# Kernel optimization log

Hardware: AMD Instinct MI355X
Metric: run time of the kernel (lower is better)

## Reference

```python
import jax, jax.numpy as jnp
import numpy as np

N, E = 50000, 800000
IN_DIM, HID, OUT_DIM, HEADS = 256, 128, 128, 2
EPS_BN = 1e-5


def _glorot(key, shape):
    fan_in, fan_out = shape[0], shape[-1]
    lim = float(np.sqrt(6.0 / (fan_in + fan_out)))
    return jax.random.uniform(key, shape, jnp.float32, -lim, lim)


def setup_inputs() -> dict:
    key = jax.random.key(0)
    ks = jax.random.split(key, 12)
    x = jax.random.normal(ks[0], (N, IN_DIM), jnp.float32)
    edge_index = jax.random.randint(ks[1], (2, E), 0, N, jnp.int64)
    return {
        "x": x,
        "edge_index": edge_index,
        # layer 1 (heads=2, concat)
        "W1": _glorot(ks[2], (IN_DIM, HEADS * HID)),
        "att_src1": _glorot(ks[3], (HEADS, HID)),
        "att_dst1": _glorot(ks[4], (HEADS, HID)),
        "b1": jnp.zeros((HEADS * HID,), jnp.float32),
        "g1": jnp.ones((HEADS * HID,), jnp.float32),
        "be1": jnp.zeros((HEADS * HID,), jnp.float32),
        # layer 2 (heads=1, no concat)
        "W2": _glorot(ks[5], (HEADS * HID, OUT_DIM)),
        "att_src2": _glorot(ks[6], (1, OUT_DIM)),
        "att_dst2": _glorot(ks[7], (1, OUT_DIM)),
        "b2": jnp.zeros((OUT_DIM,), jnp.float32),
        "g2": jnp.ones((OUT_DIM,), jnp.float32),
        "be2": jnp.zeros((OUT_DIM,), jnp.float32),
    }


def gat_conv(x, src, dst, W, att_src, att_dst, bias, heads, out_ch, concat):
    """PyG GATConv forward (dropout=identity at eval). Messages flow src->dst,
    softmax over incoming edges of dst, sum-aggregate."""
    h = (x @ W).reshape(-1, heads, out_ch)             # [N, H, C]
    a_s = jnp.einsum('nhc,hc->nh', h, att_src)          # [N, H]
    a_d = jnp.einsum('nhc,hc->nh', h, att_dst)
    e = jax.nn.leaky_relu(a_s[src] + a_d[dst], 0.2)     # [E, H]
    m = jax.ops.segment_max(e, dst, num_segments=N)     # [N, H]
    m = jnp.where(jnp.isfinite(m), m, 0.0)
    w = jnp.exp(e - m[dst])                             # [E, H]
    denom = jax.ops.segment_sum(w, dst, num_segments=N) # [N, H]
    alpha = w / (denom[dst] + 1e-16)                    # [E, H]
    msg = h[src] * alpha[:, :, None]                    # [E, H, C]
    out = jax.ops.segment_sum(msg, dst, num_segments=N) # [N, H, C]
    if concat:
        out = out.reshape(-1, heads * out_ch)
    else:
        out = out.mean(axis=1)
    return out + bias


def batchnorm_relu(x, gamma, beta):
    mu = x.mean(axis=0)
    var = x.var(axis=0)  # biased, as used for normalization in torch BN
    xn = (x - mu) * jax.lax.rsqrt(var + EPS_BN)
    return jax.nn.relu(xn * gamma + beta)


def reference(x, edge_index, W1, att_src1, att_dst1, b1, g1, be1,
              W2, att_src2, att_dst2, b2, g2, be2):
    src, dst = edge_index[0], edge_index[1]
    h = gat_conv(x, src, dst, W1, att_src1, att_dst1, b1, HEADS, HID, True)
    h = batchnorm_relu(h, g1, be1)
    h = gat_conv(h, src, dst, W2, att_src2, att_dst2, b2, 1, OUT_DIM, False)
    h = batchnorm_relu(h, g2, be2)
    return h
```

## Files before the change

### kernel.cpp

```cpp
#include <hip/hip_runtime.h>
#include <math.h>

#define IN_DIM 256
#define EPS_BN 1e-5f
#define NS 16

typedef __attribute__((ext_vector_type(8))) short short8v;
typedef __attribute__((ext_vector_type(4))) float f32x4;

__device__ __forceinline__ float lrelu(float v) { return v > 0.f ? v : 0.2f * v; }

__device__ __forceinline__ unsigned short f2bf(float f) {
    unsigned int u = __float_as_uint(f);
    u += 0x7fffu + ((u >> 16) & 1u);
    return (unsigned short)(u >> 16);
}
__device__ __forceinline__ float bf2f(unsigned short s) {
    return __uint_as_float((unsigned int)s << 16);
}

__device__ __forceinline__ void gld16(const void* g, void* l) {
    __builtin_amdgcn_global_load_lds((const __attribute__((address_space(1))) void*)g,
                                     (__attribute__((address_space(3))) void*)l, 16, 0, 0);
}

__device__ __forceinline__ int edge_at(const void* ei, int is64, long long i) {
    if (is64) return (int)((const long long*)ei)[i];
    return ((const int*)ei)[i];
}

__global__ __launch_bounds__(256) void prep_kernel(const float* __restrict__ x,
                                                   unsigned short* __restrict__ xb, long long n8,
                                                   const float* __restrict__ W1,
                                                   unsigned short* __restrict__ Wt1,
                                                   const float* __restrict__ W2,
                                                   unsigned short* __restrict__ Wt2,
                                                   const unsigned int* __restrict__ eiw,
                                                   int* __restrict__ flag, long long nwords) {
    __shared__ int nz;
    long long nbx = (n8 + 255) / 256;
    long long b = blockIdx.x;
    if (b < nbx) {
        long long i = b * 256 + threadIdx.x;
        if (i < n8) {
            const float4* p = (const float4*)(x + i * 8);
            float4 v0 = p[0], v1 = p[1];
            ushort4 o0, o1;
            o0.x = f2bf(v0.x); o0.y = f2bf(v0.y); o0.z = f2bf(v0.z); o0.w = f2bf(v0.w);
            o1.x = f2bf(v1.x); o1.y = f2bf(v1.y); o1.z = f2bf(v1.z); o1.w = f2bf(v1.w);
            *(ushort4*)(xb + i * 8) = o0;
            *(ushort4*)(xb + i * 8 + 4) = o1;
        }
        return;
    }
    b -= nbx;
    if (b < 256) {
        int idx = (int)b * 256 + threadIdx.x;
        int c = idx >> 8, k = idx & 255;
        Wt1[idx] = f2bf(W1[(long long)k * 256 + c]);
        return;
    }
    b -= 256;
    if (b < 128) {
        int idx = (int)b * 256 + threadIdx.x;
        int c = idx >> 8, k = idx & 255;
        Wt2[idx] = f2bf(W2[(long long)k * 128 + c]);
        return;
    }
    if (threadIdx.x == 0) nz = 0;
    __syncthreads();
    int cnt = 0;
    for (int i = 0; i < 4; i++) {
        long long idx = 2LL * (threadIdx.x + i * 256) + 1;
        if (idx < nwords && eiw[idx] != 0u) cnt++;
    }
    if (cnt) atomicAdd(&nz, 1);
    __syncthreads();
    if (threadIdx.x == 0) flag[0] = (nz == 0) ? 1 : 0;
}

__global__ void count_deg_kernel(const void* __restrict__ ei, const int* __restrict__ flag,
                                 int* __restrict__ deg, int E_) {
    int is64 = flag[0];
    int i = blockIdx.x * 256 + threadIdx.x;
    if (i < E_) {
        int d = edge_at(ei, is64, (long long)E_ + i);
        atomicAdd(&deg[d], 1);
    }
}

__global__ __launch_bounds__(256) void scan_partial_kernel(const int* __restrict__ deg,
                                                           int* __restrict__ bsum, int n) {
    __shared__ int sh[256];
    int t = threadIdx.x;
    int i = blockIdx.x * 256 + t;
    sh[t] = (i < n) ? deg[i] : 0;
    __syncthreads();
    for (int off = 128; off >= 1; off >>= 1) {
        if (t < off) sh[t] += sh[t + off];
        __syncthreads();
    }
    if (t == 0) bsum[blockIdx.x] = sh[0];
}

__global__ __launch_bounds__(256) void scan_write_kernel(const int* __restrict__ deg,
                                                         const int* __restrict__ bsum,
                                                         int* __restrict__ rowptr,
                                                         int* __restrict__ ctr, int n, int nb) {
    __shared__ int sh[256];
    __shared__ int base_sh;
    int t = threadIdx.x;
    int b = blockIdx.x;
    sh[t] = (t < b) ? bsum[t] : 0;
    __syncthreads();
    for (int off = 128; off >= 1; off >>= 1) {
        if (t < off) sh[t] += sh[t + off];
        __syncthreads();
    }
    if (t == 0) base_sh = sh[0];
    __syncthreads();
    int i = b * 256 + t;
    int d = (i < n) ? deg[i] : 0;
    sh[t] = d;
    __syncthreads();
    for (int off = 1; off < 256; off <<= 1) {
        int u = (t >= off) ? sh[t - off] : 0;
        __syncthreads();
        sh[t] += u;
        __syncthreads();
    }
    if (i < n) {
        int v = base_sh + sh[t] - d;
        rowptr[i] = v;
        ctr[i] = v;
    }
    if (b == nb - 1 && t == 255) rowptr[n] = base_sh + sh[255];
}

__global__ void scatter_kernel(const void* __restrict__ ei, const int* __restrict__ flag,
                               int* __restrict__ ctr, int* __restrict__ srcs, int E_) {
    int is64 = flag[0];
    int i = blockIdx.x * 256 + threadIdx.x;
    if (i < E_) {
        int s = edge_at(ei, is64, i);
        int d = edge_at(ei, is64, (long long)E_ + i);
        int pos = atomicAdd(&ctr[d], 1);
        srcs[pos] = s;
    }
}

template <int NCOL, int NH, bool FUSEBN>
__global__ __launch_bounds__(256) void gemm_mfma_kernel(const unsigned short* __restrict__ Ab,
                                                        const unsigned short* __restrict__ Wt,
                                                        unsigned short* __restrict__ C,
                                                        const float* __restrict__ att_s,
                                                        const float* __restrict__ att_d,
                                                        float* __restrict__ a_s,
                                                        float* __restrict__ a_d, int M,
                                                        const float* __restrict__ bnsh,
                                                        const float* __restrict__ gamma,
                                                        const float* __restrict__ beta) {
    __shared__ unsigned short B_lds[64 * 256];
    __shared__ unsigned short A_lds[128 * 64];
    __shared__ float scs[FUSEBN ? 256 : 1];
    __shared__ float shs[FUSEBN ? 256 : 1];
    const int t = threadIdx.x;
    const int w = t >> 6, l = t & 63;
    const int row0 = blockIdx.x * 128;
    const int col0 = blockIdx.y * 64;

    {
        const char* wb = (const char*)Wt + (size_t)col0 * 512;
#pragma unroll
        for (int it = 0; it < 8; ++it) {
            int q = w * 8 + it;
            int i = q * 64 + l;
            int r = i >> 5;
            int cs = (i & 31) ^ (r & 7);
            gld16(wb + (size_t)r * 512 + cs * 16, (char*)B_lds + q * 1024);
        }
    }

    short8v nxt[4];
    const char* ab = (const char*)Ab + (size_t)row0 * 512;

    if (FUSEBN) {
        {
            int c = t;
            float s = 0.f, q = 0.f;
#pragma unroll
            for (int sh = 0; sh < NS; sh++) { s += bnsh[sh * 512 + c]; q += bnsh[sh * 512 + 256 + c]; }
            float invN = 1.f / (float)M;
            float mu = s * invN;
            float var = q * invN - mu * mu;
            float sc = rsqrtf(var + EPS_BN) * gamma[c];
            scs[c] = sc;
            shs[c] = beta[c] - mu * sc;
        }
#pragma unroll
        for (int it = 0; it < 4; ++it) {
            int i = it * 256 + t;
            int r = i >> 3, g = i & 7;
            int gr = row0 + r;
            nxt[it] = (gr < M) ? *(const short8v*)(Ab + (size_t)gr * 256 + g * 8)
                               : (short8v)(short)0;
        }
        __syncthreads();
#pragma unroll
        for (int it = 0; it < 4; ++it) {
            int i = it * 256 + t;
            int r = i >> 3, g = i & 7;
            int kb = g * 8;
            float4 s0 = *(const float4*)&scs[kb], s1 = *(const float4*)&scs[kb + 4];
            float4 h0 = *(const float4*)&shs[kb], h1 = *(const float4*)&shs[kb + 4];
            short8v v = nxt[it];
            short8v ov;
            ov[0] = (short)f2bf(fmaxf(bf2f((unsigned short)v[0]) * s0.x + h0.x, 0.f));
            ov[1] = (short)f2bf(fmaxf(bf2f((unsigned short)v[1]) * s0.y + h0.y, 0.f));
            ov[2] = (short)f2bf(fmaxf(bf2f((unsigned short)v[2]) * s0.z + h0.z, 0.f));
            ov[3] = (short)f2bf(fmaxf(bf2f((unsigned short)v[3]) * s0.w + h0.w, 0.f));
            ov[4] = (short)f2bf(fmaxf(bf2f((unsigned short)v[4]) * s1.x + h1.x, 0.f));
            ov[5] = (short)f2bf(fmaxf(bf2f((unsigned short)v[5]) * s1.y + h1.y, 0.f));
            ov[6] = (short)f2bf(fmaxf(bf2f((unsigned short)v[6]) * s1.z + h1.z, 0.f));
            ov[7] = (short)f2bf(fmaxf(bf2f((unsigned short)v[7]) * s1.w + h1.w, 0.f));
            *(short8v*)((char*)A_lds + r * 128 + ((g ^ (r & 7)) << 4)) = ov;
        }
    } else {
#pragma unroll
        for (int it = 0; it < 4; ++it) {
            int q = w * 4 + it;
            int i = q * 64 + l;
            int r = i >> 3;
            int cs = (i & 7) ^ (r & 7);
            gld16(ab + (size_t)r * 512 + cs * 16, (char*)A_lds + q * 1024);
        }
    }
    __syncthreads();

    const int rl = l & 15, kg = l >> 4;
    f32x4 acc0[4], acc1[4];
#pragma unroll
    for (int i = 0; i < 4; ++i) { acc0[i] = (f32x4)(0.f); acc1[i] = (f32x4)(0.f); }

    const int ar0 = w * 32 + rl, ar1 = ar0 + 16;
    const int aswz = (ar0 & 7) << 4;

    for (int c = 0; c < 4; ++c) {
        if (FUSEBN && c < 3) {
#pragma unroll
            for (int it = 0; it < 4; ++it) {
                int i = it * 256 + t;
                int r = i >> 3, g = i & 7;
                int gr = row0 + r;
                nxt[it] = (gr < M) ? *(const short8v*)(Ab + (size_t)gr * 256 + (c + 1) * 64 + g * 8)
                                   : (short8v)(short)0;
            }
        }
#pragma unroll
        for (int s = 0; s < 2; ++s) {
            short8v a0 = *(const short8v*)((const char*)A_lds +
                          ((ar0 * 128 + s * 64 + kg * 16) ^ aswz));
            short8v a1 = *(const short8v*)((const char*)A_lds +
                          ((ar1 * 128 + s * 64 + kg * 16) ^ aswz));
#pragma unroll
            for (int ct = 0; ct < 4; ++ct) {
                int br = ct * 16 + rl;
                short8v bfr = *(const short8v*)((const char*)B_lds +
                               ((br * 512 + c * 128 + s * 64 + kg * 16) ^ ((br & 7) << 4)));
                acc0[ct] = __builtin_amdgcn_mfma_f32_16x16x32_bf16(a0, bfr, acc0[ct], 0, 0, 0);
                acc1[ct] = __builtin_amdgcn_mfma_f32_16x16x32_bf16(a1, bfr, acc1[ct], 0, 0, 0);
            }
        }
        __syncthreads();
        if (c < 3) {
            if (FUSEBN) {
#pragma unroll
                for (int it = 0; it < 4; ++it) {
                    int i = it * 256 + t;
                    int r = i >> 3, g = i & 7;
                    int kb = (c + 1) * 64 + g * 8;
                    float4 s0 = *(const float4*)&scs[kb], s1 = *(const float4*)&scs[kb + 4];
                    float4 h0 = *(const float4*)&shs[kb], h1 = *(const float4*)&shs[kb + 4];
                    short8v v = nxt[it];
                    short8v ov;
                    ov[0] = (short)f2bf(fmaxf(bf2f((unsigned short)v[0]) * s0.x + h0.x, 0.f));
                    ov[1] = (short)f2bf(fmaxf(bf2f((unsigned short)v[1]) * s0.y + h0.y, 0.f));
                    ov[2] = (short)f2bf(fmaxf(bf2f((unsigned short)v[2]) * s0.z + h0.z, 0.f));
                    ov[3] = (short)f2bf(fmaxf(bf2f((unsigned short)v[3]) * s0.w + h0.w, 0.f));
                    ov[4] = (short)f2bf(fmaxf(bf2f((unsigned short)v[4]) * s1.x + h1.x, 0.f));
                    ov[5] = (short)f2bf(fmaxf(bf2f((unsigned short)v[5]) * s1.y + h1.y, 0.f));
                    ov[6] = (short)f2bf(fmaxf(bf2f((unsigned short)v[6]) * s1.z + h1.z, 0.f));
                    ov[7] = (short)f2bf(fmaxf(bf2f((unsigned short)v[7]) * s1.w + h1.w, 0.f));
                    *(short8v*)((char*)A_lds + r * 128 + ((g ^ (r & 7)) << 4)) = ov;
                }
            } else {
#pragma unroll
                for (int it = 0; it < 4; ++it) {
                    int q = w * 4 + it;
                    int i = q * 64 + l;
                    int r = i >> 3;
                    int cs = (i & 7) ^ (r & 7);
                    gld16(ab + (size_t)r * 512 + (c + 1) * 128 + cs * 16, (char*)A_lds + q * 1024);
                }
            }
            __syncthreads();
        }
    }

#pragma unroll
    for (int ct = 0; ct < 4; ++ct) {
#pragma unroll
        for (int r = 0; r < 4; ++r) {
            int gr0 = row0 + w * 32 + kg * 4 + r;
            if (gr0 < M) C[(long long)gr0 * NCOL + col0 + ct * 16 + rl] = f2bf(acc0[ct][r]);
            int gr1 = gr0 + 16;
            if (gr1 < M) C[(long long)gr1 * NCOL + col0 + ct * 16 + rl] = f2bf(acc1[ct][r]);
        }
    }

    float asp0[4] = {}, adp0[4] = {}, asp1[4] = {}, adp1[4] = {};
#pragma unroll
    for (int ct = 0; ct < 4; ++ct) {
        int col = col0 + ct * 16 + rl;
        float vs = att_s[col], vd = att_d[col];
#pragma unroll
        for (int r = 0; r < 4; ++r) {
            asp0[r] += acc0[ct][r] * vs; adp0[r] += acc0[ct][r] * vd;
            asp1[r] += acc1[ct][r] * vs; adp1[r] += acc1[ct][r] * vd;
        }
    }
#pragma unroll
    for (int off = 1; off < 16; off <<= 1) {
#pragma unroll
        for (int r = 0; r < 4; ++r) {
            asp0[r] += __shfl_xor(asp0[r], off);
            adp0[r] += __shfl_xor(adp0[r], off);
            asp1[r] += __shfl_xor(asp1[r], off);
            adp1[r] += __shfl_xor(adp1[r], off);
        }
    }
    if (rl == 0) {
        int head = (NH == 2) ? (col0 >> 7) : 0;
#pragma unroll
        for (int r = 0; r < 4; ++r) {
            int gr0 = row0 + w * 32 + kg * 4 + r;
            if (gr0 < M) {
                atomicAdd(&a_s[gr0 * NH + head], asp0[r]);
                atomicAdd(&a_d[gr0 * NH + head], adp0[r]);
            }
            int gr1 = gr0 + 16;
            if (gr1 < M) {
                atomicAdd(&a_s[gr1 * NH + head], asp1[r]);
                atomicAdd(&a_d[gr1 * NH + head], adp1[r]);
            }
        }
    }
}

__global__ __launch_bounds__(256) void aggregate1_kernel(const unsigned short* __restrict__ h,
                                                         const int* __restrict__ rowptr,
                                                         const int* __restrict__ srcs,
                                                         const float* __restrict__ a_s,
                                                         const float* __restrict__ a_d,
                                                         const float* __restrict__ bias,
                                                         unsigned short* __restrict__ out,
                                                         float* __restrict__ bnsh, int Nn) {
    __shared__ float sw_lds[4 * 256];
    __shared__ float ssum[4][256];
    __shared__ float ssq[4][256];
    const int t = threadIdx.x;
    const int wid = t >> 6, lane = t & 63;
    const int n = blockIdx.x * 4 + wid;
    const int colb = (lane & 31) * 8;
    if (lane < 32) {
#pragma unroll
        for (int j = 0; j < 8; j++) { ssum[wid][colb + j] = 0.f; ssq[wid][colb + j] = 0.f; }
    }
    if (n < Nn) {
        float* wbase = &sw_lds[wid * 256];
        int beg = rowptr[n], end = rowptr[n + 1];
        float2 adv = *(const float2*)&a_d[(size_t)n * 2];
        float ad0 = adv.x, ad1 = adv.y;
        const int hh = (lane >> 4) & 1;
        const int eb = lane >> 5;
        float acc[8] = {0.f, 0.f, 0.f, 0.f, 0.f, 0.f, 0.f, 0.f};
        float den = 0.f, m0 = -1e30f, m1 = -1e30f;

        for (int cb = beg; cb < end; cb += 64) {
            int cnt = end - cb; if (cnt > 64) cnt = 64;
            float e0 = -1e30f, e1 = -1e30f;
            int s_l = 0;
            if (lane < cnt) {
                s_l = srcs[cb + lane];
                float2 av = *(const float2*)&a_s[(size_t)s_l * 2];
                e0 = lrelu(av.x + ad0);
                e1 = lrelu(av.y + ad1);
            }
            float cm0 = e0, cm1 = e1;
            for (int off = 32; off >= 1; off >>= 1) {
                cm0 = fmaxf(cm0, __shfl_xor(cm0, off));
                cm1 = fmaxf(cm1, __shfl_xor(cm1, off));
            }
            if (cm0 > m0 || cm1 > m1) {
                float f0 = (cm0 > m0) ? __expf(m0 - cm0) : 1.f;
                float f1 = (cm1 > m1) ? __expf(m1 - cm1) : 1.f;
                m0 = fmaxf(m0, cm0); m1 = fmaxf(m1, cm1);
                float fo = hh ? f1 : f0;
#pragma unroll
                for (int j = 0; j < 8; j++) acc[j] *= fo;
                den *= fo;
            }
            if (lane < cnt) {
                *(float2*)&wbase[lane * 2] = make_float2(__int_as_float(s_l), __expf(e0 - m0));
                *(float2*)&wbase[128 + lane * 2] = make_float2(__int_as_float(s_l), __expf(e1 - m1));
            }
            int c = 0;
            for (; c + 8 <= cnt; c += 8) {
                float2 sw0 = *(const float2*)&wbase[hh * 128 + (c + eb) * 2];
                float2 sw1 = *(const float2*)&wbase[hh * 128 + (c + 2 + eb) * 2];
                float2 sw2 = *(const float2*)&wbase[hh * 128 + (c + 4 + eb) * 2];
                float2 sw3 = *(const float2*)&wbase[hh * 128 + (c + 6 + eb) * 2];
                short8v p0 = *(const short8v*)(h + ((size_t)__float_as_int(sw0.x) << 8) + colb);
                short8v p1 = *(const short8v*)(h + ((size_t)__float_as_int(sw1.x) << 8) + colb);
                short8v p2 = *(const short8v*)(h + ((size_t)__float_as_int(sw2.x) << 8) + colb);
                short8v p3 = *(const short8v*)(h + ((size_t)__float_as_int(sw3.x) << 8) + colb);
                den += sw0.y + sw1.y + sw2.y + sw3.y;
#pragma unroll
                for (int j = 0; j < 8; j++)
                    acc[j] += sw0.y * bf2f((unsigned short)p0[j]) + sw1.y * bf2f((unsigned short)p1[j])
                            + sw2.y * bf2f((unsigned short)p2[j]) + sw3.y * bf2f((unsigned short)p3[j]);
            }
            for (; c + 4 <= cnt; c += 4) {
                float2 sw0 = *(const float2*)&wbase[hh * 128 + (c + eb) * 2];
                float2 sw1 = *(const float2*)&wbase[hh * 128 + (c + 2 + eb) * 2];
                short8v p0 = *(const short8v*)(h + ((size_t)__float_as_int(sw0.x) << 8) + colb);
                short8v p1 = *(const short8v*)(h + ((size_t)__float_as_int(sw1.x) << 8) + colb);
                den += sw0.y + sw1.y;
#pragma unroll
                for (int j = 0; j < 8; j++)
                    acc[j] += sw0.y * bf2f((unsigned short)p0[j]) + sw1.y * bf2f((unsigned short)p1[j]);
            }
            for (; c < cnt; c += 2) {
                int e = c + eb;
                if (e < cnt) {
                    float2 sw0 = *(const float2*)&wbase[hh * 128 + e * 2];
                    short8v p0 = *(const short8v*)(h + ((size_t)__float_as_int(sw0.x) << 8) + colb);
                    den += sw0.y;
#pragma unroll
                    for (int j = 0; j < 8; j++) acc[j] += sw0.y * bf2f((unsigned short)p0[j]);
                }
            }
        }
        den += __shfl_xor(den, 32);
#pragma unroll
        for (int j = 0; j < 8; j++) acc[j] += __shfl_xor(acc[j], 32);
        if (lane < 32) {
            float inv = 1.f / (den + 1e-16f);
            float4 b0 = *(const float4*)&bias[colb];
            float4 b1 = *(const float4*)&bias[colb + 4];
            float of[8];
            of[0] = acc[0] * inv + b0.x; of[1] = acc[1] * inv + b0.y;
            of[2] = acc[2] * inv + b0.z; of[3] = acc[3] * inv + b0.w;
            of[4] = acc[4] * inv + b1.x; of[5] = acc[5] * inv + b1.y;
            of[6] = acc[6] * inv + b1.z; of[7] = acc[7] * inv + b1.w;
            short8v o;
#pragma unroll
            for (int j = 0; j < 8; j++) {
                o[j] = (short)f2bf(of[j]);
                ssum[wid][colb + j] = of[j];
                ssq[wid][colb + j] = of[j] * of[j];
            }
            *(short8v*)(out + ((size_t)n << 8) + colb) = o;
        }
    }
    __syncthreads();
    {
        int sh = blockIdx.x & (NS - 1);
        float s = ssum[0][t] + ssum[1][t] + ssum[2][t] + ssum[3][t];
        float q = ssq[0][t] + ssq[1][t] + ssq[2][t] + ssq[3][t];
        atomicAdd(&bnsh[sh * 512 + t], s);
        atomicAdd(&bnsh[sh * 512 + 256 + t], q);
    }
}

__global__ __launch_bounds__(256) void aggregate2_kernel(const unsigned short* __restrict__ h,
                                                         const int* __restrict__ rowptr,
                                                         const int* __restrict__ srcs,
                                                         const float* __restrict__ a_s,
                                                         const float* __restrict__ a_d,
                                                         const float* __restrict__ bias,
                                                         float* __restrict__ out,
                                                         float* __restrict__ bnsh, int Nn) {
    __shared__ float sw_lds[4 * 128];
    __shared__ float ssum[4][128];
    __shared__ float ssq[4][128];
    const int t = threadIdx.x;
    const int wid = t >> 6, lane = t & 63;
    const int n = blockIdx.x * 4 + wid;
    const int colb = (lane & 15) * 8;
    if (lane < 16) {
#pragma unroll
        for (int j = 0; j < 8; j++) { ssum[wid][colb + j] = 0.f; ssq[wid][colb + j] = 0.f; }
    }
    if (n < Nn) {
        float* wbase = &sw_lds[wid * 128];
        int beg = rowptr[n], end = rowptr[n + 1];
        float ad = a_d[n];
        const int eo = lane >> 4;
        float acc[8] = {0.f, 0.f, 0.f, 0.f, 0.f, 0.f, 0.f, 0.f};
        float den = 0.f, m = -1e30f;

        for (int cb = beg; cb < end; cb += 64) {
            int cnt = end - cb; if (cnt > 64) cnt = 64;
            float e_ = -1e30f;
            int s_l = 0;
            if (lane < cnt) {
                s_l = srcs[cb + lane];
                e_ = lrelu(a_s[s_l] + ad);
            }
            float cm = e_;
            for (int off = 32; off >= 1; off >>= 1) cm = fmaxf(cm, __shfl_xor(cm, off));
            if (cm > m) {
                float f = __expf(m - cm);
                m = cm;
#pragma unroll
                for (int j = 0; j < 8; j++) acc[j] *= f;
                den *= f;
            }
            if (lane < cnt)
                *(float2*)&wbase[lane * 2] = make_float2(__int_as_float(s_l), __expf(e_ - m));
            int c = 0;
            for (; c + 16 <= cnt; c += 16) {
                float2 sw0 = *(const float2*)&wbase[(c + eo) * 2];
                float2 sw1 = *(const float2*)&wbase[(c + 4 + eo) * 2];
                float2 sw2 = *(const float2*)&wbase[(c + 8 + eo) * 2];
                float2 sw3 = *(const float2*)&wbase[(c + 12 + eo) * 2];
                short8v p0 = *(const short8v*)(h + ((size_t)__float_as_int(sw0.x) << 7) + colb);
                short8v p1 = *(const short8v*)(h + ((size_t)__float_as_int(sw1.x) << 7) + colb);
                short8v p2 = *(const short8v*)(h + ((size_t)__float_as_int(sw2.x) << 7) + colb);
                short8v p3 = *(const short8v*)(h + ((size_t)__float_as_int(sw3.x) << 7) + colb);
                den += sw0.y + sw1.y + sw2.y + sw3.y;
#pragma unroll
                for (int j = 0; j < 8; j++)
                    acc[j] += sw0.y * bf2f((unsigned short)p0[j]) + sw1.y * bf2f((unsigned short)p1[j])
                            + sw2.y * bf2f((unsigned short)p2[j]) + sw3.y * bf2f((unsigned short)p3[j]);
            }
            for (; c + 8 <= cnt; c += 8) {
                float2 sw0 = *(const float2*)&wbase[(c + eo) * 2];
                float2 sw1 = *(const float2*)&wbase[(c + 4 + eo) * 2];
                short8v p0 = *(const short8v*)(h + ((size_t)__float_as_int(sw0.x) << 7) + colb);
                short8v p1 = *(const short8v*)(h + ((size_t)__float_as_int(sw1.x) << 7) + colb);
                den += sw0.y + sw1.y;
#pragma unroll
                for (int j = 0; j < 8; j++)
                    acc[j] += sw0.y * bf2f((unsigned short)p0[j]) + sw1.y * bf2f((unsigned short)p1[j]);
            }
            for (; c < cnt; c += 4) {
                int e = c + eo;
                if (e < cnt) {
                    float2 sw0 = *(const float2*)&wbase[e * 2];
                    short8v p0 = *(const short8v*)(h + ((size_t)__float_as_int(sw0.x) << 7) + colb);
                    den += sw0.y;
#pragma unroll
                    for (int j = 0; j < 8; j++) acc[j] += sw0.y * bf2f((unsigned short)p0[j]);
                }
            }
        }
        den += __shfl_xor(den, 16);
        den += __shfl_xor(den, 32);
#pragma unroll
        for (int j = 0; j < 8; j++) {
            acc[j] += __shfl_xor(acc[j], 16);
            acc[j] += __shfl_xor(acc[j], 32);
        }
        if (lane < 16) {
            float inv = 1.f / (den + 1e-16f);
            float4 b0 = *(const float4*)&bias[colb];
            float4 b1 = *(const float4*)&bias[colb + 4];
            float of[8];
            of[0] = acc[0] * inv + b0.x; of[1] = acc[1] * inv + b0.y;
            of[2] = acc[2] * inv + b0.z; of[3] = acc[3] * inv + b0.w;
            of[4] = acc[4] * inv + b1.x; of[5] = acc[5] * inv + b1.y;
            of[6] = acc[6] * inv + b1.z; of[7] = acc[7] * inv + b1.w;
#pragma unroll
            for (int j = 0; j < 8; j++) {
                ssum[wid][colb + j] = of[j];
                ssq[wid][colb + j] = of[j] * of[j];
            }
            float* ob = out + (size_t)n * 128 + colb;
            *(float4*)ob = make_float4(of[0], of[1], of[2], of[3]);
            *(float4*)(ob + 4) = make_float4(of[4], of[5], of[6], of[7]);
        }
    }
    __syncthreads();
    if (t < 128) {
        int sh = blockIdx.x & (NS - 1);
        float s = ssum[0][t] + ssum[1][t] + ssum[2][t] + ssum[3][t];
        atomicAdd(&bnsh[sh * 256 + t], s);
    } else {
        int c = t - 128;
        int sh = blockIdx.x & (NS - 1);
        float q = ssq[0][c] + ssq[1][c] + ssq[2][c] + ssq[3][c];
        atomicAdd(&bnsh[sh * 256 + 128 + c], q);
    }
}

__global__ __launch_bounds__(256) void bn_apply_final_kernel(float* __restrict__ x,
                                                             const float* __restrict__ bnsh,
                                                             const float* __restrict__ gamma,
                                                             const float* __restrict__ beta,
                                                             int Nn) {
    int t = threadIdx.x;
    int col = t & 127;
    float s = 0.f, q = 0.f;
#pragma unroll
    for (int sh = 0; sh < NS; sh++) { s += bnsh[sh * 256 + col]; q += bnsh[sh * 256 + 128 + col]; }
    float mu = s / (float)Nn;
    float var = q / (float)Nn - mu * mu;
    float sc = rsqrtf(var + EPS_BN) * gamma[col];
    float sh_ = beta[col] - mu * sc;
    int r0 = blockIdx.x * 2 + (t >> 7);
    int rs = gridDim.x * 2;
    for (int r = r0; r < Nn; r += rs) {
        size_t idx = (size_t)r * 128 + col;
        x[idx] = fmaxf(x[idx] * sc + sh_, 0.f);
    }
}

extern "C" void kernel_launch(void* const* d_in, const int* in_sizes, int n_in,
                              void* d_out, int out_size, void* d_ws, size_t ws_size,
                              hipStream_t stream) {
    const float* x        = (const float*)d_in[0];
    const void*  ei       = d_in[1];
    const float* W1       = (const float*)d_in[2];
    const float* att_src1 = (const float*)d_in[3];
    const float* att_dst1 = (const float*)d_in[4];
    const float* b1       = (const float*)d_in[5];
    const float* g1       = (const float*)d_in[6];
    const float* be1      = (const float*)d_in[7];
    const float* W2       = (const float*)d_in[8];
    const float* att_src2 = (const float*)d_in[9];
    const float* att_dst2 = (const float*)d_in[10];
    const float* b2       = (const float*)d_in[11];
    const float* g2       = (const float*)d_in[12];
    const float* be2      = (const float*)d_in[13];

    const int Nn = in_sizes[0] / IN_DIM;
    const int E_ = in_sizes[1] / 2;
    const int gb = (Nn + 127) / 128;
    const int Mpad = gb * 128 + 128;

    char* ws = (char*)d_ws;
    size_t o = 0;
    auto alloc = [&](size_t bytes) {
        size_t r = o;
        o += (bytes + 255) & ~(size_t)255;
        return r;
    };
    int* flag = (int*)(ws + alloc(4));
    size_t z0 = o;
    int*   deg   = (int*)(ws + alloc((size_t)Nn * 4));
    float* as1   = (float*)(ws + alloc((size_t)Nn * 2 * 4));
    float* ad1   = (float*)(ws + alloc((size_t)Nn * 2 * 4));
    float* as2   = (float*)(ws + alloc((size_t)Nn * 4));
    float* ad2   = (float*)(ws + alloc((size_t)Nn * 4));
    float* bn1sh = (float*)(ws + alloc((size_t)NS * 512 * 4));
    float* bn2sh = (float*)(ws + alloc((size_t)NS * 256 * 4));
    size_t z1 = o;
    int*   rowptr = (int*)(ws + alloc((size_t)(Nn + 1) * 4));
    int*   ctr    = (int*)(ws + alloc((size_t)Nn * 4));
    int*   srcs   = (int*)(ws + alloc((size_t)E_ * 4));
    int*   bsum   = (int*)(ws + alloc(256 * 4));
    unsigned short* Wt1  = (unsigned short*)(ws + alloc((size_t)256 * 256 * 2));
    unsigned short* Wt2  = (unsigned short*)(ws + alloc((size_t)128 * 256 * 2));
    unsigned short* xb   = (unsigned short*)(ws + alloc((size_t)Mpad * 256 * 2));
    unsigned short* x2b0 = (unsigned short*)(ws + alloc((size_t)Nn * 256 * 2));
    unsigned short* h1b  = (unsigned short*)(ws + alloc((size_t)Nn * 256 * 2));
    unsigned short* h2b  = (unsigned short*)(ws + alloc((size_t)Nn * 128 * 2));
    float* outf = (float*)d_out;

    hipMemsetAsync(ws + z0, 0, z1 - z0, stream);

    {
        long long n8 = (long long)Nn * 256 / 8;
        long long grid = (n8 + 255) / 256 + 256 + 128 + 1;
        prep_kernel<<<(int)grid, 256, 0, stream>>>(x, xb, n8, W1, Wt1, W2, Wt2,
                                                   (const unsigned int*)ei, flag,
                                                   (long long)2 * E_);
    }

    int eb = (E_ + 255) / 256;
    int nsb = (Nn + 255) / 256;
    count_deg_kernel<<<eb, 256, 0, stream>>>(ei, flag, deg, E_);
    scan_partial_kernel<<<nsb, 256, 0, stream>>>(deg, bsum, Nn);
    scan_write_kernel<<<nsb, 256, 0, stream>>>(deg, bsum, rowptr, ctr, Nn, nsb);
    scatter_kernel<<<eb, 256, 0, stream>>>(ei, flag, ctr, srcs, E_);

    int nb4 = (Nn + 3) / 4;

    gemm_mfma_kernel<256, 2, false><<<dim3(gb, 4), 256, 0, stream>>>(
        xb, Wt1, h1b, att_src1, att_dst1, as1, ad1, Nn, nullptr, nullptr, nullptr);
    aggregate1_kernel<<<nb4, 256, 0, stream>>>(h1b, rowptr, srcs, as1, ad1, b1, x2b0, bn1sh, Nn);

    gemm_mfma_kernel<128, 1, true><<<dim3(gb, 2), 256, 0, stream>>>(
        x2b0, Wt2, h2b, att_src2, att_dst2, as2, ad2, Nn, bn1sh, g1, be1);
    aggregate2_kernel<<<nb4, 256, 0, stream>>>(h2b, rowptr, srcs, as2, ad2, b2, outf, bn2sh, Nn);
    bn_apply_final_kernel<<<512, 256, 0, stream>>>(outf, bn2sh, g2, be2, Nn);
}
```

Baseline: 306.2 us.

## Use grid-stride persistent blocks in aggregation kernels with register BN partials

Both aggregation kernels become grid-stride loops over destination nodes, launched with a fixed 2048 blocks instead of one block per four nodes. Each lane keeps its batch-norm sum and sum-of-squares partials in registers across its nodes and does the LDS reduction and global atomics once per block. This cuts global atomic traffic on the sharded BN buffers by roughly 6x and removes per-node shared-memory staging. It reuses the weight LDS buffer for the reduction, which adds extra barriers at the end, and it can leave some blocks with more work than others when node degrees vary.

```diff
diff --git a/kernel.cpp b/kernel.cpp
--- a/kernel.cpp
+++ b/kernel.cpp
@@ -365,24 +365,20 @@
                                                          const float* __restrict__ bias,
                                                          unsigned short* __restrict__ out,
                                                          float* __restrict__ bnsh, int Nn) {
-    __shared__ float sw_lds[4 * 256];
-    __shared__ float ssum[4][256];
-    __shared__ float ssq[4][256];
+    __shared__ float sw_lds[4][256];
     const int t = threadIdx.x;
     const int wid = t >> 6, lane = t & 63;
-    const int n = blockIdx.x * 4 + wid;
+    const int hh = (lane >> 4) & 1;
+    const int eb = lane >> 5;
     const int colb = (lane & 31) * 8;
-    if (lane < 32) {
-#pragma unroll
-        for (int j = 0; j < 8; j++) { ssum[wid][colb + j] = 0.f; ssq[wid][colb + j] = 0.f; }
-    }
-    if (n < Nn) {
-        float* wbase = &sw_lds[wid * 256];
+    float* wbase = sw_lds[wid];
+    float bnsum[8] = {}, bnsq[8] = {};
+    const int stride = gridDim.x * 4;
+
+    for (int n = blockIdx.x * 4 + wid; n < Nn; n += stride) {
         int beg = rowptr[n], end = rowptr[n + 1];
         float2 adv = *(const float2*)&a_d[(size_t)n * 2];
         float ad0 = adv.x, ad1 = adv.y;
-        const int hh = (lane >> 4) & 1;
-        const int eb = lane >> 5;
         float acc[8] = {0.f, 0.f, 0.f, 0.f, 0.f, 0.f, 0.f, 0.f};
         float den = 0.f, m0 = -1e30f, m1 = -1e30f;
 
@@ -467,19 +463,34 @@
 #pragma unroll
             for (int j = 0; j < 8; j++) {
                 o[j] = (short)f2bf(of[j]);
-                ssum[wid][colb + j] = of[j];
-                ssq[wid][colb + j] = of[j] * of[j];
+                bnsum[j] += of[j];
+                bnsq[j] += of[j] * of[j];
             }
             *(short8v*)(out + ((size_t)n << 8) + colb) = o;
         }
     }
+
+    __syncthreads();
+    if (lane < 32) {
+#pragma unroll
+        for (int j = 0; j < 8; j++) wbase[colb + j] = bnsum[j];
+    }
     __syncthreads();
     {
-        int sh = blockIdx.x & (NS - 1);
-        float s = ssum[0][t] + ssum[1][t] + ssum[2][t] + ssum[3][t];
-        float q = ssq[0][t] + ssq[1][t] + ssq[2][t] + ssq[3][t];
-        atomicAdd(&bnsh[sh * 512 + t], s);
-        atomicAdd(&bnsh[sh * 512 + 256 + t], q);
+        int sh = (blockIdx.x & (NS - 1)) * 512;
+        float s = sw_lds[0][t] + sw_lds[1][t] + sw_lds[2][t] + sw_lds[3][t];
+        atomicAdd(&bnsh[sh + t], s);
+    }
+    __syncthreads();
+    if (lane < 32) {
+#pragma unroll
+        for (int j = 0; j < 8; j++) wbase[colb + j] = bnsq[j];
+    }
+    __syncthreads();
+    {
+        int sh = (blockIdx.x & (NS - 1)) * 512;
+        float q = sw_lds[0][t] + sw_lds[1][t] + sw_lds[2][t] + sw_lds[3][t];
+        atomicAdd(&bnsh[sh + 256 + t], q);
     }
 }
 
@@ -491,22 +502,18 @@
                                                          const float* __restrict__ bias,
                                                          float* __restrict__ out,
                                                          float* __restrict__ bnsh, int Nn) {
-    __shared__ float sw_lds[4 * 128];
-    __shared__ float ssum[4][128];
-    __shared__ float ssq[4][128];
+    __shared__ float sw_lds[4][128];
     const int t = threadIdx.x;
     const int wid = t >> 6, lane = t & 63;
-    const int n = blockIdx.x * 4 + wid;
+    const int eo = lane >> 4;
     const int colb = (lane & 15) * 8;
-    if (lane < 16) {
-#pragma unroll
-        for (int j = 0; j < 8; j++) { ssum[wid][colb + j] = 0.f; ssq[wid][colb + j] = 0.f; }
-    }
-    if (n < Nn) {
-        float* wbase = &sw_lds[wid * 128];
+    float* wbase = sw_lds[wid];
+    float bnsum[8] = {}, bnsq[8] = {};
+    const int stride = gridDim.x * 4;
+
+    for (int n = blockIdx.x * 4 + wid; n < Nn; n += stride) {
         int beg = rowptr[n], end = rowptr[n + 1];
         float ad = a_d[n];
-        const int eo = lane >> 4;
         float acc[8] = {0.f, 0.f, 0.f, 0.f, 0.f, 0.f, 0.f, 0.f};
         float den = 0.f, m = -1e30f;
 
@@ -584,24 +591,36 @@
             of[6] = acc[6] * inv + b1.z; of[7] = acc[7] * inv + b1.w;
 #pragma unroll
             for (int j = 0; j < 8; j++) {
-                ssum[wid][colb + j] = of[j];
-                ssq[wid][colb + j] = of[j] * of[j];
+                bnsum[j] += of[j];
+                bnsq[j] += of[j] * of[j];
             }
             float* ob = out + (size_t)n * 128 + colb;
             *(float4*)ob = make_float4(of[0], of[1], of[2], of[3]);
             *(float4*)(ob + 4) = make_float4(of[4], of[5], of[6], of[7]);
         }
     }
+
+    __syncthreads();
+    if (lane < 16) {
+#pragma unroll
+        for (int j = 0; j < 8; j++) wbase[colb + j] = bnsum[j];
+    }
     __syncthreads();
     if (t < 128) {
-        int sh = blockIdx.x & (NS - 1);
-        float s = ssum[0][t] + ssum[1][t] + ssum[2][t] + ssum[3][t];
-        atomicAdd(&bnsh[sh * 256 + t], s);
-    } else {
-        int c = t - 128;
-        int sh = blockIdx.x & (NS - 1);
-        float q = ssq[0][c] + ssq[1][c] + ssq[2][c] + ssq[3][c];
-        atomicAdd(&bnsh[sh * 256 + 128 + c], q);
+        int sh = (blockIdx.x & (NS - 1)) * 256;
+        float s = sw_lds[0][t] + sw_lds[1][t] + sw_lds[2][t] + sw_lds[3][t];
+        atomicAdd(&bnsh[sh + t], s);
+    }
+    __syncthreads();
+    if (lane < 16) {
+#pragma unroll
+        for (int j = 0; j < 8; j++) wbase[colb + j] = bnsq[j];
+    }
+    __syncthreads();
+    if (t < 128) {
+        int sh = (blockIdx.x & (NS - 1)) * 256;
+        float q = sw_lds[0][t] + sw_lds[1][t] + sw_lds[2][t] + sw_lds[3][t];
+        atomicAdd(&bnsh[sh + 128 + t], q);
     }
 }
 
@@ -696,14 +715,16 @@
     scan_write_kernel<<<nsb, 256, 0, stream>>>(deg, bsum, rowptr, ctr, Nn, nsb);
     scatter_kernel<<<eb, 256, 0, stream>>>(ei, flag, ctr, srcs, E_);
 
-    int nb4 = (Nn + 3) / 4;
+    const int agg_blocks = 2048;
 
     gemm_mfma_kernel<256, 2, false><<<dim3(gb, 4), 256, 0, stream>>>(
         xb, Wt1, h1b, att_src1, att_dst1, as1, ad1, Nn, nullptr, nullptr, nullptr);
-    aggregate1_kernel<<<nb4, 256, 0, stream>>>(h1b, rowptr, srcs, as1, ad1, b1, x2b0, bn1sh, Nn);
+    aggregate1_kernel<<<agg_blocks, 256, 0, stream>>>(h1b, rowptr, srcs, as1, ad1, b1, x2b0,
+                                                      bn1sh, Nn);
 
     gemm_mfma_kernel<128, 1, true><<<dim3(gb, 2), 256, 0, stream>>>(
         x2b0, Wt2, h2b, att_src2, att_dst2, as2, ad2, Nn, bn1sh, g1, be1);
-    aggregate2_kernel<<<nb4, 256, 0, stream>>>(h2b, rowptr, srcs, as2, ad2, b2, outf, bn2sh, Nn);
+    aggregate2_kernel<<<agg_blocks, 256, 0, stream>>>(h2b, rowptr, srcs, as2, ad2, b2, outf,
+                                                      bn2sh, Nn);
     bn_apply_final_kernel<<<512, 256, 0, stream>>>(outf, bn2sh, g2, be2, Nn);
 }
```

After: 295.6 us. 1.04x faster.
